# Kernel optimization log

Hardware: AMD Instinct MI355X
Metric: run time of the kernel (lower is better)

Reference implementation:

```python
import jax, jax.numpy as jnp
import numpy as np

B, SEQ, D_TOK = 2, 2048, 1536
H, DH = 24, 64
TP, NS, NMH, DFLOW = 4, 256, 8, 64


def setup_inputs() -> dict:
    key = jax.random.key(0)
    ks = jax.random.split(key, 10)
    s = 0.02  # weight scale to keep activations sane
    return {
        "hidden_states": jax.random.normal(ks[0], (B, SEQ, D_TOK), jnp.float32),
        "Wq": jax.random.normal(ks[1], (D_TOK, D_TOK), jnp.float32) * s,
        "Wk": jax.random.normal(ks[2], (D_TOK, D_TOK), jnp.float32) * s,
        "Wv": jax.random.normal(ks[3], (D_TOK, D_TOK), jnp.float32) * s,
        "Wo": jax.random.normal(ks[4], (D_TOK, D_TOK), jnp.float32) * s,
        "bo": jnp.zeros((D_TOK,), jnp.float32),
        "M": jax.random.normal(ks[5], (B, TP, NS, DFLOW), jnp.float32),
        "W_region": jax.random.uniform(ks[6], (B, TP, NS, 1), jnp.float32),
        "Fk": jax.random.normal(ks[7], (NMH, DFLOW, DH), jnp.float32) * s,
        "Fv": jax.random.normal(ks[8], (NMH, DFLOW, DH), jnp.float32) * s,
    }


def reference(hidden_states, Wq, Wk, Wv, Wo, bo, M, W_region, Fk, Fv):
    # QKV projections, split into heads: [B, H, seq, Dh]
    Q = (hidden_states @ Wq).reshape(B, SEQ, H, DH).transpose(0, 2, 1, 3)
    K = (hidden_states @ Wk).reshape(B, SEQ, H, DH).transpose(0, 2, 1, 3)
    V = (hidden_states @ Wv).reshape(B, SEQ, H, DH).transpose(0, 2, 1, 3)

    # Motion injection (vectorized over b, h, t): region-gated flow deltas
    # delta[b,h,t,n,d] = W_region[b,t,n] * (M[b,t,n,:] @ Fk[h])
    gate = W_region[:, None]  # [B,1,TP,NS,1]
    dK = jnp.einsum('btnf,hfd->bhtnd', M, Fk) * gate  # [B,NMH,TP,NS,DH]
    dV = jnp.einsum('btnf,hfd->bhtnd', M, Fv) * gate

    # seq = 2 blocks (content, canny) x TP frames x NS spatial tokens;
    # delta is applied to both halves of each frame, first NMH heads only.
    K = K.reshape(B, H, 2, TP, NS, DH).at[:, :NMH].add(dK[:, :, None]).reshape(B, H, SEQ, DH)
    V = V.reshape(B, H, 2, TP, NS, DH).at[:, :NMH].add(dV[:, :, None]).reshape(B, H, SEQ, DH)

    # Standard SDPA
    scale = 1.0 / np.sqrt(DH).astype(np.float32)
    scores = jnp.einsum('bhqd,bhkd->bhqk', Q, K) * scale
    attn_w = jax.nn.softmax(scores, axis=-1)
    out = jnp.einsum('bhqk,bhkd->bhqd', attn_w, V)

    out = out.transpose(0, 2, 1, 3).reshape(B, SEQ, D_TOK)
    return out @ Wo + bo
```

## Files before the change

### kernel.cpp

```cpp
#include <hip/hip_runtime.h>
#include <hip/hip_bf16.h>

typedef __attribute__((ext_vector_type(4))) float f32x4;
typedef __attribute__((ext_vector_type(8))) short bf16x8;

#define LOG2E 1.4426950408889634f

__device__ __forceinline__ unsigned short f2b(float f) {
  union { float f; unsigned u; } v; v.f = f;
  unsigned r = v.u + 0x7fffu + ((v.u >> 16) & 1u);
  return (unsigned short)(r >> 16);
}
__device__ __forceinline__ float b2f(unsigned short s) {
  union { unsigned u; float f; } v; v.u = ((unsigned)s) << 16;
  return v.f;
}
__device__ __forceinline__ unsigned cvtpk(float lo, float hi) {
  unsigned r;
  asm("v_cvt_pk_bf16_f32 %0, %1, %2" : "=v"(r) : "v"(lo), "v"(hi));
  return r;
}
__device__ __forceinline__ float fexp2(float x) {
  float r;
  asm("v_exp_f32 %0, %1" : "=v"(r) : "v"(x));
  return r;
}

__device__ __forceinline__ void gload_lds16(const void* g, void* l) {
  __builtin_amdgcn_global_load_lds(
      (const __attribute__((address_space(1))) unsigned*)g,
      (__attribute__((address_space(3))) unsigned*)l, 16, 0, 0);
}

__global__ __launch_bounds__(256) void k_cvt(const float* __restrict__ src,
                                             unsigned short* __restrict__ dst, int n4) {
  int i = blockIdx.x * 256 + threadIdx.x;
  if (i >= n4) return;
  float4 v = ((const float4*)src)[i];
  ushort4 o;
  o.x = f2b(v.x); o.y = f2b(v.y); o.z = f2b(v.z); o.w = f2b(v.w);
  ((ushort4*)dst)[i] = o;
}

__global__ __launch_bounds__(256) void k_transpose3(const float* __restrict__ s0,
                                                    const float* __restrict__ s1,
                                                    const float* __restrict__ s2,
                                                    unsigned short* __restrict__ dst) {
  __shared__ float tile[64][65];
  const int which = blockIdx.x / 576;
  const int bid = blockIdx.x % 576;
  const float* src = which == 0 ? s0 : (which == 1 ? s1 : s2);
  unsigned short* d = dst + (size_t)which * 1536 * 1536;
  const int tx = threadIdx.x & 63, ty = threadIdx.x >> 6;
  const int r0 = (bid / 24) * 64, c0 = (bid % 24) * 64;
#pragma unroll
  for (int j = 0; j < 16; ++j)
    tile[ty + j * 4][tx] = src[(size_t)(r0 + ty + j * 4) * 1536 + c0 + tx];
  __syncthreads();
#pragma unroll
  for (int j = 0; j < 16; ++j)
    d[(size_t)(c0 + ty + j * 4) * 1536 + r0 + tx] = f2b(tile[tx][ty + j * 4]);
}

__global__ __launch_bounds__(256) void k_transpose(const float* __restrict__ src,
                                                   unsigned short* __restrict__ dst) {
  __shared__ float tile[64][65];
  const int tx = threadIdx.x & 63, ty = threadIdx.x >> 6;
  const int r0 = (blockIdx.x / 24) * 64, c0 = (blockIdx.x % 24) * 64;
#pragma unroll
  for (int j = 0; j < 16; ++j)
    tile[ty + j * 4][tx] = src[(size_t)(r0 + ty + j * 4) * 1536 + c0 + tx];
  __syncthreads();
#pragma unroll
  for (int j = 0; j < 16; ++j)
    dst[(size_t)(c0 + ty + j * 4) * 1536 + r0 + tx] = f2b(tile[tx][ty + j * 4]);
}

template <int OUTBF16>
__global__ __launch_bounds__(256) void k_gemm(const unsigned short* __restrict__ A,
                                              const unsigned short* __restrict__ BT,
                                              void* __restrict__ C,
                                              const float* __restrict__ bias,
                                              int M, int N, int K, int gridN) {
  __shared__ unsigned short As[128 * 32];
  __shared__ unsigned short Bs[128 * 32];
  const int tid = threadIdx.x;
  const int lane = tid & 63, wave = tid >> 6;
  const int bm = (blockIdx.x / gridN) * 128;
  const int bn = (blockIdx.x % gridN) * 128;
  const int wr = (wave >> 1) * 64, wc = (wave & 1) * 64;
  const int r15 = lane & 15, g = lane >> 4;
  const int row0 = tid >> 2, c0 = tid & 3;

  f32x4 acc[4][4] = {};

  for (int k0 = 0; k0 < K; k0 += 32) {
    __syncthreads();
    gload_lds16(A + (size_t)(bm + row0) * K + k0 + c0 * 8, (char*)As + wave * 1024);
    gload_lds16(A + (size_t)(bm + row0 + 64) * K + k0 + c0 * 8,
                (char*)As + 4096 + wave * 1024);
    gload_lds16(BT + (size_t)(bn + row0) * K + k0 + c0 * 8, (char*)Bs + wave * 1024);
    gload_lds16(BT + (size_t)(bn + row0 + 64) * K + k0 + c0 * 8,
                (char*)Bs + 4096 + wave * 1024);
    __syncthreads();
    bf16x8 af[4], bfr[4];
#pragma unroll
    for (int m = 0; m < 4; ++m) {
      af[m] = *(const bf16x8*)&As[(wr + m * 16 + r15) * 32 + g * 8];
      bfr[m] = *(const bf16x8*)&Bs[(wc + m * 16 + r15) * 32 + g * 8];
    }
#pragma unroll
    for (int m = 0; m < 4; ++m)
#pragma unroll
      for (int n = 0; n < 4; ++n)
        acc[m][n] = __builtin_amdgcn_mfma_f32_16x16x32_bf16(af[m], bfr[n], acc[m][n], 0, 0, 0);
  }

#pragma unroll
  for (int m = 0; m < 4; ++m)
#pragma unroll
    for (int n = 0; n < 4; ++n)
#pragma unroll
      for (int i = 0; i < 4; ++i) {
        int row = bm + wr + m * 16 + g * 4 + i;
        int col = bn + wc + n * 16 + r15;
        float v = acc[m][n][i];
        if (OUTBF16)
          ((unsigned short*)C)[(size_t)row * N + col] = f2b(v);
        else
          ((float*)C)[(size_t)row * N + col] = v + bias[col];
      }
}

__global__ __launch_bounds__(256) void k_inject(const float* __restrict__ Mm,
                                                const float* __restrict__ Wr,
                                                const float* __restrict__ Fk,
                                                const float* __restrict__ Fv,
                                                unsigned short* __restrict__ qkv) {
  __shared__ float Ml[256];
  __shared__ float gl[4];
  const int bid = blockIdx.x;
  const int nb = bid & 63, t = (bid >> 6) & 3, h = (bid >> 8) & 7, b = bid >> 11;
  const int tid = threadIdx.x;
  const int nl = tid >> 6, d = tid & 63;
  Ml[tid] = Mm[(size_t)(((b * 4 + t) * 256 + nb * 4) * 64) + tid];
  if (tid < 4) gl[tid] = Wr[(b * 4 + t) * 256 + nb * 4 + tid];
  __syncthreads();
  float ak = 0.f, av = 0.f;
#pragma unroll 8
  for (int f = 0; f < 64; ++f) {
    float mv = Ml[nl * 64 + f];
    ak += mv * Fk[(h * 64 + f) * 64 + d];
    av += mv * Fv[(h * 64 + f) * 64 + d];
  }
  float gate = gl[nl];
  ak *= gate; av *= gate;
  const int n = nb * 4 + nl;
  const size_t s0 = (size_t)(b * 2048 + t * 256 + n);
#pragma unroll
  for (int r = 0; r < 2; ++r) {
    size_t row = s0 + (size_t)r * 1024;
    size_t ik = row * 4608 + 1536 + h * 64 + d;
    qkv[ik] = f2b(b2f(qkv[ik]) + ak);
    size_t iv = row * 4608 + 3072 + h * 64 + d;
    qkv[iv] = f2b(b2f(qkv[iv]) + av);
  }
}

__global__ __launch_bounds__(256, 3) void k_attn(const unsigned short* __restrict__ qkv,
                                                 unsigned short* __restrict__ attno) {
  __shared__ unsigned short Kl[2 * 64 * 64];
  __shared__ unsigned short VT[2 * 64 * 72];
  __shared__ unsigned short Pl[4 * 32 * 72];
  const int tid = threadIdx.x;
  const int lane = tid & 63, wave = tid >> 6;
  const int bid = blockIdx.x;
  const int qt = bid & 15;
  const int h = (bid >> 4) % 24;
  const int b = (bid >> 4) / 24;
  const int r15 = lane & 15, g = lane >> 4;
  const int q0 = qt * 128 + wave * 32;
  const size_t RS = 4608;
  const size_t tokbase = (size_t)(b * 2048);
  unsigned short* Plw = Pl + wave * 32 * 72;

  bf16x8 qb[2][2];
  {
    const float qs = 0.125f * LOG2E;
#pragma unroll
    for (int qh = 0; qh < 2; ++qh) {
      const unsigned short* qrow = qkv + (tokbase + q0 + qh * 16 + r15) * RS + h * 64;
#pragma unroll
      for (int kk = 0; kk < 2; ++kk) {
        bf16x8 v = *(const bf16x8*)(qrow + kk * 32 + g * 8);
#pragma unroll
        for (int e = 0; e < 8; ++e)
          v[e] = (short)f2b(b2f((unsigned short)v[e]) * qs);
        qb[qh][kk] = v;
      }
    }
  }

  f32x4 o[2][4] = {};
  float m_run[2] = {-1e30f, -1e30f}, l_run[2] = {0.f, 0.f};
  bf16x8 vr[2];

  const int ch0 = wave * 2 * 64 + lane, ch1 = (wave * 2 + 1) * 64 + lane;
  const int kr0 = ch0 >> 3, kc0s = ((ch0 & 7) ^ (kr0 & 7)) * 8;
  const int kr1 = ch1 >> 3, kc1s = ((ch1 & 7) ^ (kr1 & 7)) * 8;

#define STAGE_K(buf, kv0)                                                          \
  {                                                                                \
    gload_lds16(qkv + (tokbase + (kv0) + kr0) * RS + 1536 + h * 64 + kc0s,         \
                (char*)Kl + (buf) * 8192 + (wave * 2) * 1024);                     \
    gload_lds16(qkv + (tokbase + (kv0) + kr1) * RS + 1536 + h * 64 + kc1s,         \
                (char*)Kl + (buf) * 8192 + (wave * 2 + 1) * 1024);                 \
  }
#define LOAD_V(kv0)                                                                \
  {                                                                                \
    const unsigned short* vrow = qkv + (tokbase + (kv0) + lane) * RS + 3072 + h * 64; \
    vr[0] = *(const bf16x8*)(vrow + (wave * 2) * 8);                               \
    vr[1] = *(const bf16x8*)(vrow + (wave * 2 + 1) * 8);                           \
  }
#define WRITE_V(buf)                                                               \
  {                                                                                \
    _Pragma("unroll") for (int s = 0; s < 2; ++s) {                                \
      int d0 = (wave * 2 + s) * 8;                                                 \
      _Pragma("unroll") for (int e = 0; e < 8; ++e)                                \
          VT[(buf) * 4608 + (d0 + e) * 72 + lane] = (unsigned short)vr[s][e];      \
    }                                                                              \
  }

  STAGE_K(0, 0);
  LOAD_V(0);
  asm volatile("s_waitcnt vmcnt(0)" ::: "memory");
  WRITE_V(0);
  __syncthreads();

  int cur = 0;
  for (int t = 0; t < 32; ++t) {
    const int kv0 = t * 64;
    if (t < 31) {
      STAGE_K(cur ^ 1, kv0 + 64);
      LOAD_V(kv0 + 64);
    }

    f32x4 st[4][2];
    const unsigned short* Kb = Kl + cur * 4096;
    __builtin_amdgcn_s_setprio(1);
#pragma unroll
    for (int m = 0; m < 4; ++m) {
      int row = m * 16 + r15;
      int r7 = row & 7;
      bf16x8 ka0 = *(const bf16x8*)&Kb[row * 64 + ((g ^ r7) * 8)];
      bf16x8 ka1 = *(const bf16x8*)&Kb[row * 64 + (((4 + g) ^ r7) * 8)];
#pragma unroll
      for (int qh = 0; qh < 2; ++qh) {
        f32x4 z = {0.f, 0.f, 0.f, 0.f};
        st[m][qh] = __builtin_amdgcn_mfma_f32_16x16x32_bf16(ka0, qb[qh][0], z, 0, 0, 0);
        st[m][qh] = __builtin_amdgcn_mfma_f32_16x16x32_bf16(ka1, qb[qh][1], st[m][qh], 0, 0, 0);
      }
    }
    __builtin_amdgcn_s_setprio(0);

    float pm[2];
#pragma unroll
    for (int qh = 0; qh < 2; ++qh) {
      float p = fmaxf(fmaxf(fmaxf(st[0][qh][0], st[0][qh][1]), fmaxf(st[0][qh][2], st[0][qh][3])),
                      fmaxf(fmaxf(st[1][qh][0], st[1][qh][1]), fmaxf(st[1][qh][2], st[1][qh][3])));
      p = fmaxf(p,
                fmaxf(fmaxf(fmaxf(st[2][qh][0], st[2][qh][1]), fmaxf(st[2][qh][2], st[2][qh][3])),
                      fmaxf(fmaxf(st[3][qh][0], st[3][qh][1]), fmaxf(st[3][qh][2], st[3][qh][3]))));
      p = fmaxf(p, __shfl_xor(p, 16, 64));
      pm[qh] = fmaxf(p, __shfl_xor(p, 32, 64));
    }

    if (!__all(pm[0] - m_run[0] <= 8.0f && pm[1] - m_run[1] <= 8.0f)) {
#pragma unroll
      for (int qh = 0; qh < 2; ++qh) {
        float mnew = fmaxf(m_run[qh], pm[qh]);
        float fac = fexp2(m_run[qh] - mnew);
        l_run[qh] *= fac;
        float f_i[4];
#pragma unroll
        for (int i = 0; i < 4; ++i)
          f_i[i] = __shfl(fac, (lane & 48) | ((((lane >> 4) & 3) << 2) + i), 64);
#pragma unroll
        for (int dt = 0; dt < 4; ++dt)
#pragma unroll
          for (int i = 0; i < 4; ++i) o[qh][dt][i] *= f_i[i];
        m_run[qh] = mnew;
      }
    }

    float psum[2] = {0.f, 0.f};
#pragma unroll
    for (int m = 0; m < 4; ++m)
#pragma unroll
      for (int qh = 0; qh < 2; ++qh) {
        float p0 = fexp2(st[m][qh][0] - m_run[qh]);
        float p1 = fexp2(st[m][qh][1] - m_run[qh]);
        float p2 = fexp2(st[m][qh][2] - m_run[qh]);
        float p3 = fexp2(st[m][qh][3] - m_run[qh]);
        psum[qh] += (p0 + p1) + (p2 + p3);
        uint2 w2;
        w2.x = cvtpk(p0, p1);
        w2.y = cvtpk(p2, p3);
        *(uint2*)&Plw[(qh * 16 + r15) * 72 + m * 16 + g * 4] = w2;
      }
#pragma unroll
    for (int qh = 0; qh < 2; ++qh) {
      psum[qh] += __shfl_xor(psum[qh], 16, 64);
      psum[qh] += __shfl_xor(psum[qh], 32, 64);
      l_run[qh] += psum[qh];
    }

    const unsigned short* Vb = VT + cur * 4608;
    __builtin_amdgcn_s_setprio(1);
#pragma unroll
    for (int kap = 0; kap < 2; ++kap) {
      bf16x8 pa0 = *(const bf16x8*)&Plw[(r15) * 72 + kap * 32 + g * 8];
      bf16x8 pa1 = *(const bf16x8*)&Plw[(16 + r15) * 72 + kap * 32 + g * 8];
#pragma unroll
      for (int dt = 0; dt < 4; ++dt) {
        bf16x8 vb = *(const bf16x8*)&Vb[(dt * 16 + r15) * 72 + kap * 32 + g * 8];
        o[0][dt] = __builtin_amdgcn_mfma_f32_16x16x32_bf16(pa0, vb, o[0][dt], 0, 0, 0);
        o[1][dt] = __builtin_amdgcn_mfma_f32_16x16x32_bf16(pa1, vb, o[1][dt], 0, 0, 0);
      }
    }
    __builtin_amdgcn_s_setprio(0);

    if (t < 31) {
      asm volatile("s_waitcnt vmcnt(0)" ::: "memory");
      WRITE_V(cur ^ 1);
    }
    __syncthreads();
    cur ^= 1;
  }

#pragma unroll
  for (int qh = 0; qh < 2; ++qh) {
    float rl = 1.0f / l_run[qh];
    float r_i[4];
#pragma unroll
    for (int i = 0; i < 4; ++i)
      r_i[i] = __shfl(rl, (lane & 48) | ((((lane >> 4) & 3) << 2) + i), 64);
#pragma unroll
    for (int dt = 0; dt < 4; ++dt)
#pragma unroll
      for (int i = 0; i < 4; ++i) {
        int q = q0 + qh * 16 + ((lane >> 4) << 2) + i;
        int col = h * 64 + dt * 16 + r15;
        attno[(tokbase + q) * 1536 + col] = f2b(o[qh][dt][i] * r_i[i]);
      }
  }
}

extern "C" void kernel_launch(void* const* d_in, const int* in_sizes, int n_in,
                              void* d_out, int out_size, void* d_ws, size_t ws_size,
                              hipStream_t stream) {
  const float* hs = (const float*)d_in[0];
  const float* Wq = (const float*)d_in[1];
  const float* Wk = (const float*)d_in[2];
  const float* Wv = (const float*)d_in[3];
  const float* Wo = (const float*)d_in[4];
  const float* bo = (const float*)d_in[5];
  const float* Mm = (const float*)d_in[6];
  const float* Wr = (const float*)d_in[7];
  const float* Fk = (const float*)d_in[8];
  const float* Fv = (const float*)d_in[9];
  float* out = (float*)d_out;

  unsigned short* hsb   = (unsigned short*)d_ws;
  unsigned short* wqkvt = hsb + (size_t)4096 * 1536;
  unsigned short* qkv   = wqkvt + (size_t)4608 * 1536;
  unsigned short* attno = hsb;
  unsigned short* wot   = wqkvt;

  k_cvt<<<6144, 256, 0, stream>>>(hs, hsb, 1572864);
  k_transpose3<<<1728, 256, 0, stream>>>(Wq, Wk, Wv, wqkvt);

  k_gemm<1><<<32 * 36, 256, 0, stream>>>(hsb, wqkvt, (void*)qkv, (const float*)nullptr,
                                         4096, 4608, 1536, 36);
  k_transpose<<<576, 256, 0, stream>>>(Wo, wot);
  k_inject<<<4096, 256, 0, stream>>>(Mm, Wr, Fk, Fv, qkv);
  k_attn<<<768, 256, 0, stream>>>(qkv, attno);
  k_gemm<0><<<32 * 12, 256, 0, stream>>>(attno, wot, (void*)out, bo, 4096, 1536, 1536, 12);
}
```

Measured before the change: 252.3 us.

## Replace QKV GEMM with 256x256-tile, 8-wave, pipelined, swizzled-LDS kernel

Adds a new GEMM kernel for the QKV projection. It uses 256x256 output tiles with 512 threads and double-buffered async global-to-LDS loads that are staggered across four phases per K step. LDS reads use an XOR swizzle, blocks are remapped per XCD, and barriers with priority hints interleave MFMA with loads. The intent is more data reuse per tile and loads hidden behind compute, replacing the simple 128x128 kernel that synchronises on every step. The cost is higher register pressure and a tail effect from launching only 288 blocks.

After: 282.3 us. 11.9% more time.

```diff
diff --git a/kernel.cpp b/kernel.cpp
--- a/kernel.cpp
+++ b/kernel.cpp
@@ -25,11 +25,13 @@
   asm("v_exp_f32 %0, %1" : "=v"(r) : "v"(x));
   return r;
 }
-
 __device__ __forceinline__ void gload_lds16(const void* g, void* l) {
   __builtin_amdgcn_global_load_lds(
       (const __attribute__((address_space(1))) unsigned*)g,
       (__attribute__((address_space(3))) unsigned*)l, 16, 0, 0);
+}
+__device__ __forceinline__ f32x4 mfma16(bf16x8 a, bf16x8 b, f32x4 c) {
+  return __builtin_amdgcn_mfma_f32_16x16x32_bf16(a, b, c, 0, 0, 0);
 }
 
 __global__ __launch_bounds__(256) void k_cvt(const float* __restrict__ src,
@@ -74,6 +76,136 @@
 #pragma unroll
   for (int j = 0; j < 16; ++j)
     dst[(size_t)(c0 + ty + j * 4) * 1536 + r0 + tx] = f2b(tile[tx][ty + j * 4]);
+}
+
+__global__ __launch_bounds__(512, 2) void k_gemm8(const unsigned short* __restrict__ A,
+                                                  const unsigned short* __restrict__ BT,
+                                                  unsigned short* __restrict__ C,
+                                                  int M, int N, int K, int gridN) {
+  __shared__ unsigned short As[16384];
+  __shared__ unsigned short Bs[16384];
+  const int tid = threadIdx.x;
+  const int lane = tid & 63, wave = tid >> 6;
+  const int wm = wave >> 2, wn = wave & 3;
+  const int r15 = lane & 15, g = lane >> 4;
+  int bid = blockIdx.x;
+  {
+    int cpx = gridDim.x >> 3;
+    bid = (bid & 7) * cpx + (bid >> 3);
+  }
+  const int bm = (bid / gridN) * 256;
+  const int bn = (bid % gridN) * 256;
+  const int NT = K >> 5;
+
+  const int srow = tid >> 2;
+  const int slc = (tid & 3) ^ ((srow >> 1) & 3);
+
+  f32x4 acc[8][4] = {};
+
+  auto STAGE = [&](int tl, int part) {
+    const bool isB = part >= 2;
+    const unsigned short* src = isB ? BT : A;
+    const int rb = (isB ? bn : bm) + (part & 1) * 128;
+    char* db = (char*)(isB ? Bs : As) + ((tl & 1) * 2 + (part & 1)) * 8192 + wave * 1024;
+    gload_lds16(src + (size_t)(rb + srow) * K + tl * 32 + slc * 8, db);
+  };
+
+  STAGE(0, 0); STAGE(0, 1); STAGE(0, 2); STAGE(0, 3);
+  STAGE(1, 2); STAGE(1, 0); STAGE(1, 1);
+  asm volatile("s_waitcnt vmcnt(3)" ::: "memory");
+  __builtin_amdgcn_s_barrier();
+
+  bf16x8 af[4], bf[4];
+  for (int t = 0; t < NT; ++t) {
+    const int d = t & 1;
+    const unsigned short* Ah = As + (d * 2 + wm) * 4096;
+    const unsigned short* Bh = Bs + (d * 2 + (wn >> 1)) * 4096;
+    const int bro = (wn & 1) * 64;
+
+#pragma unroll
+    for (int j = 0; j < 4; ++j) {
+      int r = j * 16 + r15;
+      af[j] = *(const bf16x8*)&Ah[r * 32 + ((g ^ ((r >> 1) & 3)) * 8)];
+    }
+#pragma unroll
+    for (int n = 0; n < 2; ++n) {
+      int r = bro + n * 16 + r15;
+      bf[n] = *(const bf16x8*)&Bh[r * 32 + ((g ^ ((r >> 1) & 3)) * 8)];
+    }
+    if (t + 1 < NT) STAGE(t + 1, 3);
+    __builtin_amdgcn_s_barrier();
+    asm volatile("s_waitcnt lgkmcnt(0)" ::: "memory");
+    __builtin_amdgcn_sched_barrier(0);
+    __builtin_amdgcn_s_setprio(1);
+#pragma unroll
+    for (int j = 0; j < 4; ++j) {
+      acc[j][0] = mfma16(af[j], bf[0], acc[j][0]);
+      acc[j][1] = mfma16(af[j], bf[1], acc[j][1]);
+    }
+    __builtin_amdgcn_s_setprio(0);
+    __builtin_amdgcn_s_barrier();
+
+#pragma unroll
+    for (int n = 2; n < 4; ++n) {
+      int r = bro + n * 16 + r15;
+      bf[n] = *(const bf16x8*)&Bh[r * 32 + ((g ^ ((r >> 1) & 3)) * 8)];
+    }
+    __builtin_amdgcn_s_barrier();
+    asm volatile("s_waitcnt lgkmcnt(0)" ::: "memory");
+    __builtin_amdgcn_sched_barrier(0);
+    __builtin_amdgcn_s_setprio(1);
+#pragma unroll
+    for (int j = 0; j < 4; ++j) {
+      acc[j][2] = mfma16(af[j], bf[2], acc[j][2]);
+      acc[j][3] = mfma16(af[j], bf[3], acc[j][3]);
+    }
+    __builtin_amdgcn_s_setprio(0);
+    __builtin_amdgcn_s_barrier();
+
+#pragma unroll
+    for (int j = 0; j < 4; ++j) {
+      int r = 64 + j * 16 + r15;
+      af[j] = *(const bf16x8*)&Ah[r * 32 + ((g ^ ((r >> 1) & 3)) * 8)];
+    }
+    if (t + 2 < NT) STAGE(t + 2, 2);
+    __builtin_amdgcn_s_barrier();
+    asm volatile("s_waitcnt lgkmcnt(0)" ::: "memory");
+    __builtin_amdgcn_sched_barrier(0);
+    __builtin_amdgcn_s_setprio(1);
+#pragma unroll
+    for (int j = 0; j < 4; ++j) {
+      acc[4 + j][0] = mfma16(af[j], bf[0], acc[4 + j][0]);
+      acc[4 + j][1] = mfma16(af[j], bf[1], acc[4 + j][1]);
+    }
+    __builtin_amdgcn_s_setprio(0);
+    __builtin_amdgcn_s_barrier();
+
+    if (t + 2 < NT) { STAGE(t + 2, 0); STAGE(t + 2, 1); }
+    __builtin_amdgcn_s_barrier();
+    __builtin_amdgcn_s_setprio(1);
+#pragma unroll
+    for (int j = 0; j < 4; ++j) {
+      acc[4 + j][2] = mfma16(af[j], bf[2], acc[4 + j][2]);
+      acc[4 + j][3] = mfma16(af[j], bf[3], acc[4 + j][3]);
+    }
+    __builtin_amdgcn_s_setprio(0);
+    if (t < NT - 2)
+      asm volatile("s_waitcnt vmcnt(3)" ::: "memory");
+    else
+      asm volatile("s_waitcnt vmcnt(0)" ::: "memory");
+    __builtin_amdgcn_s_barrier();
+  }
+
+#pragma unroll
+  for (int m = 0; m < 8; ++m)
+#pragma unroll
+    for (int n = 0; n < 4; ++n)
+#pragma unroll
+      for (int i = 0; i < 4; ++i) {
+        int row = bm + wm * 128 + m * 16 + g * 4 + i;
+        int col = bn + wn * 64 + n * 16 + r15;
+        C[(size_t)row * N + col] = f2b(acc[m][n][i]);
+      }
 }
 
 template <int OUTBF16>
@@ -113,7 +245,7 @@
     for (int m = 0; m < 4; ++m)
 #pragma unroll
       for (int n = 0; n < 4; ++n)
-        acc[m][n] = __builtin_amdgcn_mfma_f32_16x16x32_bf16(af[m], bfr[n], acc[m][n], 0, 0, 0);
+        acc[m][n] = mfma16(af[m], bfr[n], acc[m][n]);
   }
 
 #pragma unroll
@@ -257,8 +389,8 @@
 #pragma unroll
       for (int qh = 0; qh < 2; ++qh) {
         f32x4 z = {0.f, 0.f, 0.f, 0.f};
-        st[m][qh] = __builtin_amdgcn_mfma_f32_16x16x32_bf16(ka0, qb[qh][0], z, 0, 0, 0);
-        st[m][qh] = __builtin_amdgcn_mfma_f32_16x16x32_bf16(ka1, qb[qh][1], st[m][qh], 0, 0, 0);
+        st[m][qh] = mfma16(ka0, qb[qh][0], z);
+        st[m][qh] = mfma16(ka1, qb[qh][1], st[m][qh]);
       }
     }
     __builtin_amdgcn_s_setprio(0);
@@ -324,8 +456,8 @@
 #pragma unroll
       for (int dt = 0; dt < 4; ++dt) {
         bf16x8 vb = *(const bf16x8*)&Vb[(dt * 16 + r15) * 72 + kap * 32 + g * 8];
-        o[0][dt] = __builtin_amdgcn_mfma_f32_16x16x32_bf16(pa0, vb, o[0][dt], 0, 0, 0);
-        o[1][dt] = __builtin_amdgcn_mfma_f32_16x16x32_bf16(pa1, vb, o[1][dt], 0, 0, 0);
+        o[0][dt] = mfma16(pa0, vb, o[0][dt]);
+        o[1][dt] = mfma16(pa1, vb, o[1][dt]);
       }
     }
     __builtin_amdgcn_s_setprio(0);
@@ -380,8 +512,7 @@
   k_cvt<<<6144, 256, 0, stream>>>(hs, hsb, 1572864);
   k_transpose3<<<1728, 256, 0, stream>>>(Wq, Wk, Wv, wqkvt);
 
-  k_gemm<1><<<32 * 36, 256, 0, stream>>>(hsb, wqkvt, (void*)qkv, (const float*)nullptr,
-                                         4096, 4608, 1536, 36);
+  k_gemm8<<<288, 512, 0, stream>>>(hsb, wqkvt, qkv, 4096, 4608, 1536, 18);
   k_transpose<<<576, 256, 0, stream>>>(Wo, wot);
   k_inject<<<4096, 256, 0, stream>>>(Mm, Wr, Fk, Fv, qkv);
   k_attn<<<768, 256, 0, stream>>>(qkv, attno);
```
